# Kernel optimization log

Measured on AMD Instinct MI355X. Metric: run time of the kernel, lower is better.

The kernel has to match this reference:

```python
import jax, jax.numpy as jnp
import numpy as np


def setup_inputs() -> dict:
    key = jax.random.key(0)
    k1, k2, k3, k4 = jax.random.split(key, 4)
    B, S, D_IN, D_OUT = 4, 4096, 2048, 2048
    x = jax.random.normal(k1, (B, S, D_IN), dtype=jnp.float32)
    weight = jax.random.normal(k2, (D_OUT, D_IN), dtype=jnp.float32) * 0.02
    scale_weight = jax.random.uniform(k3, (D_OUT,), dtype=jnp.float32, minval=0.5, maxval=1.5)
    bias = jax.random.normal(k4, (D_OUT,), dtype=jnp.float32) * 0.02
    return {"x": x, "weight": weight, "scale_weight": scale_weight, "bias": bias}


def reference(x, weight, scale_weight, bias):
    # FPScaledLinear.forward: cast weight to compute dtype, apply per-out-feature
    # scale (scale_weight viewed as [out, 1]), then F.linear(x, w, b).
    w = weight * scale_weight[:, None]            # [out, in]
    out = jnp.einsum('bsi,oi->bso', x, w) + bias  # [B, S, out]
    return out
```

## Files before the change

### kernel.cpp

```cpp
#include <hip/hip_runtime.h>

typedef __attribute__((ext_vector_type(8))) __bf16 bf16x8;
typedef __attribute__((ext_vector_type(4))) float f32x4;
typedef __attribute__((ext_vector_type(8))) unsigned short ushort8;
typedef const __attribute__((address_space(1))) unsigned int gq_t;
typedef __attribute__((address_space(3))) unsigned int lq_t;

__device__ __forceinline__ unsigned short f2bf(float f) {
  unsigned int u = __builtin_bit_cast(unsigned int, f);
  u += 0x7fffu + ((u >> 16) & 1u);
  return (unsigned short)(u >> 16);
}

__global__ void cvt_xw_kernel(const float* __restrict__ x, const float* __restrict__ w,
                              const float* __restrict__ scale,
                              ushort8* __restrict__ xa, ushort8* __restrict__ wb,
                              int n8x, int n8w, int k8) {
  int stride = gridDim.x * blockDim.x;
  int total = n8x + n8w;
  for (int i = blockIdx.x * blockDim.x + threadIdx.x; i < total; i += stride) {
    if (i < n8x) {
      const float4* p = (const float4*)(x) + 2 * (size_t)i;
      float4 v0 = p[0], v1 = p[1];
      ushort8 r;
      r[0] = f2bf(v0.x); r[1] = f2bf(v0.y); r[2] = f2bf(v0.z); r[3] = f2bf(v0.w);
      r[4] = f2bf(v1.x); r[5] = f2bf(v1.y); r[6] = f2bf(v1.z); r[7] = f2bf(v1.w);
      xa[i] = r;
    } else {
      int j = i - n8x;
      float s = scale[j / k8];
      const float4* p = (const float4*)(w) + 2 * (size_t)j;
      float4 v0 = p[0], v1 = p[1];
      ushort8 r;
      r[0] = f2bf(v0.x * s); r[1] = f2bf(v0.y * s); r[2] = f2bf(v0.z * s); r[3] = f2bf(v0.w * s);
      r[4] = f2bf(v1.x * s); r[5] = f2bf(v1.y * s); r[6] = f2bf(v1.z * s); r[7] = f2bf(v1.w * s);
      wb[j] = r;
    }
  }
}


#define BARRIER asm volatile("s_barrier" ::: "memory")
#define WAITV4 asm volatile("s_waitcnt vmcnt(4)" ::: "memory")
#define WAITV0 asm volatile("s_waitcnt vmcnt(0)" ::: "memory")
#define GL(p, d) __builtin_amdgcn_global_load_lds((gq_t*)(p), (lq_t*)(d), 16, 0, 0)

#define QUAD(MH, BG, NHB)                                                                \
  do {                                                                                   \
    __builtin_amdgcn_s_setprio(1);                                                       \
    _Pragma("unroll") for (int k_ = 0; k_ < 2; ++k_) {                                   \
      _Pragma("unroll") for (int mm = 0; mm < 4; ++mm) {                                 \
        _Pragma("unroll") for (int nn = 0; nn < 2; ++nn) {                               \
          acc[(MH)*4 + mm][(NHB)*2 + nn] = __builtin_amdgcn_mfma_f32_16x16x32_bf16(      \
              af[mm][k_], BG[nn][k_], acc[(MH)*4 + mm][(NHB)*2 + nn], 0, 0, 0);          \
        }                                                                                \
      }                                                                                  \
    }                                                                                    \
    __builtin_amdgcn_s_setprio(0);                                                       \
  } while (0)

#define TILE_BODY(T, CB)                                                                 \
  do {                                                                                   \
    const int t_ = (T);                                                                  \
    char* cur = lds + (CB) * 65536;                                                      \
    char* oth = lds + (((CB) ^ 1)) * 65536;                                              \
                           \
    LDA(cur, 0);                                                                         \
    if (t_ + 1 < NT) { GL(bP0lo, oth + 32768 + dstT);                                    \
                       GL(bP0hi, oth + 32768 + 8192 + dstT); }                           \
    BARRIER; QUAD(0, bg0, 0);                                                            \
                                   \
    LDB1(cur);                                                                           \
    if (t_ + 1 < NT) { GL(aP1lo, oth + 16384 + dstT);                                    \
                       GL(aP1hi, oth + 16384 + 8192 + dstT); }                           \
    BARRIER; QUAD(0, bg1, 1);                                                            \
                                   \
    LDA(cur, 1);                                                                         \
    if (t_ + 2 < NT) { GL(aP0lo, cur + dstT);                                            \
                       GL(aP0hi, cur + 8192 + dstT); }                                   \
    BARRIER; QUAD(1, bg1, 1);                                                            \
       \
    if (t_ + 2 < NT) { GL(bP1lo, cur + 49152 + dstT);                                    \
                       GL(bP1hi, cur + 49152 + 8192 + dstT); }                           \
    if (t_ == NT - 2) { WAITV0; } else { WAITV4; }                                       \
    BARRIER; QUAD(1, bg0, 0);                                                            \
    if (t_ + 1 < NT) LDB0(oth);                                                          \
    aP0lo += 64; aP0hi += 64; aP1lo += 64; aP1hi += 64;                                  \
    bP0lo += 64; bP0hi += 64; bP1lo += 64; bP1hi += 64;                                  \
  } while (0)

__global__ __launch_bounds__(512, 2) void gemm256_8ph(
    const unsigned short* __restrict__ A, const unsigned short* __restrict__ B,
    const float* __restrict__ bias, float* __restrict__ C, int M, int N, int K) {
  extern __shared__ char lds[];

  const int nbn = N >> 8;
  const int nwg = (M >> 8) * nbn;
  int bid = blockIdx.x;
  if ((nwg & 7) == 0) {
    int q = nwg >> 3;
    bid = (bid & 7) * q + (bid >> 3);
  }
  const int bm = (bid / nbn) << 8;
  const int bn = (bid % nbn) << 8;

  const int tid = threadIdx.x;
  const int lane = tid & 63;
  const int wid = tid >> 6;
  const int wr = wid >> 2;
  const int wc = wid & 3;
  const int NT = K >> 6;
  const int dstT = tid * 16;

  const int colel = (((tid & 7) ^ ((tid >> 3) & 7)) << 3);
  const unsigned short* aBase = A + (size_t)(bm + (tid >> 3)) * K + colel;
  const unsigned short* bBase = B + (size_t)(bn + ((tid >> 8) << 6) + ((tid >> 3) & 31)) * K + colel;
  const unsigned short* aP0lo = aBase;
  const unsigned short* aP0hi = aBase + (size_t)128 * K;
  const unsigned short* aP1lo = aBase + (size_t)64 * K;
  const unsigned short* aP1hi = aBase + (size_t)192 * K;
  const unsigned short* bP0lo = bBase;
  const unsigned short* bP0hi = bBase + (size_t)128 * K;
  const unsigned short* bP1lo = bBase + (size_t)32 * K;
  const unsigned short* bP1hi = bBase + (size_t)160 * K;

  const int i15 = lane & 15;
  const int qg = lane >> 4;
  const int swz = (lane & 7) << 4;
  const int colp0 = (qg << 4) ^ swz;
  const int colp1 = ((qg << 4) | 64) ^ swz;
  const int aoff = wr * 8192 + i15 * 128;
  const int boff = 32768 + wc * 4096 + i15 * 128;

  f32x4 acc[8][4];
#pragma unroll
  for (int m = 0; m < 8; ++m)
#pragma unroll
    for (int n = 0; n < 4; ++n) acc[m][n] = (f32x4){0.f, 0.f, 0.f, 0.f};

  bf16x8 af[4][2];
  bf16x8 bg0[2][2];
  bf16x8 bg1[2][2];

  auto LDA = [&](const char* base, int mh) {
    const char* p = base + mh * 16384 + aoff;
#pragma unroll
    for (int mm = 0; mm < 4; ++mm) {
      af[mm][0] = *(const bf16x8*)(p + mm * 2048 + colp0);
      af[mm][1] = *(const bf16x8*)(p + mm * 2048 + colp1);
    }
  };
  auto LDB0 = [&](const char* base) {
    const char* p = base + boff;
#pragma unroll
    for (int nn = 0; nn < 2; ++nn) {
      bg0[nn][0] = *(const bf16x8*)(p + nn * 2048 + colp0);
      bg0[nn][1] = *(const bf16x8*)(p + nn * 2048 + colp1);
    }
  };
  auto LDB1 = [&](const char* base) {
    const char* p = base + 16384 + boff;
#pragma unroll
    for (int nn = 0; nn < 2; ++nn) {
      bg1[nn][0] = *(const bf16x8*)(p + nn * 2048 + colp0);
      bg1[nn][1] = *(const bf16x8*)(p + nn * 2048 + colp1);
    }
  };

  GL(aP0lo, lds + dstT);                     GL(aP0hi, lds + 8192 + dstT);
  GL(bP1lo, lds + 49152 + dstT);             GL(bP1hi, lds + 49152 + 8192 + dstT);
  GL(bP0lo, lds + 32768 + dstT);             GL(bP0hi, lds + 32768 + 8192 + dstT);
  GL(aP1lo, lds + 16384 + dstT);             GL(aP1hi, lds + 16384 + 8192 + dstT);
  GL(aP0lo + 64, lds + 65536 + dstT);        GL(aP0hi + 64, lds + 65536 + 8192 + dstT);
  GL(bP1lo + 64, lds + 65536 + 49152 + dstT);
  GL(bP1hi + 64, lds + 65536 + 49152 + 8192 + dstT);
  WAITV4;
  BARRIER;
  LDB0(lds);
  bP0lo += 64;  bP0hi += 64;  aP1lo += 64;  aP1hi += 64;
  aP0lo += 128; aP0hi += 128; bP1lo += 128; bP1hi += 128;

  for (int t = 0; t < NT; t += 2) {
    TILE_BODY(t, 0);
    TILE_BODY(t + 1, 1);
  }

  const int r0 = bm + wr * 128 + ((lane >> 4) << 2);
  const int c0 = bn + wc * 64 + (lane & 15);
  float bv[4];
#pragma unroll
  for (int n = 0; n < 4; ++n) bv[n] = bias[c0 + n * 16];
#pragma unroll
  for (int m = 0; m < 8; ++m) {
#pragma unroll
    for (int r = 0; r < 4; ++r) {
      float* crow = C + (size_t)(r0 + m * 16 + r) * N + c0;
#pragma unroll
      for (int n = 0; n < 4; ++n) crow[n * 16] = acc[m][n][r] + bv[n];
    }
  }
}

__global__ void gemm_fallback_kernel(const float* __restrict__ X, const float* __restrict__ W,
                                     const float* __restrict__ scale, const float* __restrict__ bias,
                                     float* __restrict__ out, int M, int N, int K) {
  __shared__ float as[64][33];
  __shared__ float bs[64][33];
  int tx = threadIdx.x & 15, ty = threadIdx.x >> 4;
  int brow = blockIdx.y * 64, bcol = blockIdx.x * 64;
  float acc[4][4] = {};
  for (int k0 = 0; k0 < K; k0 += 32) {
    int kw = (K - k0 < 32) ? (K - k0) : 32;
    for (int i = 0; i < 8; ++i) {
      int idx = (int)threadIdx.x + i * 256;
      int r = idx >> 5, c = idx & 31;
      int ga = brow + r, gb = bcol + r;
      as[r][c] = (ga < M && c < kw) ? X[(size_t)ga * K + k0 + c] : 0.f;
      bs[r][c] = (gb < N && c < kw) ? W[(size_t)gb * K + k0 + c] * scale[gb] : 0.f;
    }
    __syncthreads();
    for (int k = 0; k < 32; ++k)
#pragma unroll
      for (int i = 0; i < 4; ++i)
#pragma unroll
        for (int j = 0; j < 4; ++j)
          acc[i][j] += as[ty * 4 + i][k] * bs[tx * 4 + j][k];
    __syncthreads();
  }
  for (int i = 0; i < 4; ++i) {
    int r = brow + ty * 4 + i;
    if (r >= M) continue;
    for (int j = 0; j < 4; ++j) {
      int c = bcol + tx * 4 + j;
      if (c < N) out[(size_t)r * N + c] = acc[i][j] + bias[c];
    }
  }
}

extern "C" void kernel_launch(void* const* d_in, const int* in_sizes, int n_in,
                              void* d_out, int out_size, void* d_ws, size_t ws_size,
                              hipStream_t stream) {
  const float* x     = (const float*)d_in[0];
  const float* w     = (const float*)d_in[1];
  const float* scale = (const float*)d_in[2];
  const float* bias  = (const float*)d_in[3];
  float* out = (float*)d_out;

  const long N = in_sizes[2];
  const long K = in_sizes[1] / N;
  const long M = (long)in_sizes[0] / K;

  const size_t need = ((size_t)M * K + (size_t)N * K) * sizeof(unsigned short);
  const long NT = K / 64;
  const bool ok = (ws_size >= need) && (M % 256 == 0) && (N % 256 == 0) &&
                  (K % 128 == 0) && (NT >= 4);

  if (ok) {
    unsigned short* xa = (unsigned short*)d_ws;
    unsigned short* wb = xa + (size_t)M * K;
    int n8x = (int)((size_t)M * K / 8);
    int n8w = (int)((size_t)N * K / 8);
    cvt_xw_kernel<<<2048, 256, 0, stream>>>(x, w, scale, (ushort8*)xa, (ushort8*)wb,
                                            n8x, n8w, (int)(K / 8));

    (void)hipFuncSetAttribute((const void*)gemm256_8ph,
                              hipFuncAttributeMaxDynamicSharedMemorySize, 131072);
    int nwg = (int)((M / 256) * (N / 256));
    gemm256_8ph<<<nwg, 512, 131072, stream>>>(xa, wb, bias, out, (int)M, (int)N, (int)K);
  } else {
    dim3 grid((unsigned)((N + 63) / 64), (unsigned)((M + 63) / 64));
    gemm_fallback_kernel<<<grid, 256, 0, stream>>>(x, w, scale, bias, out, (int)M, (int)N, (int)K);
  }
}
```

Before: 164.6 us.

## Halve GEMM K-tile to 32 with new LDS swizzle and smaller shared memory

Shrinks the K depth per tile from 64 to 32, which halves the LDS buffer (64KB instead of 128KB) and the per-stage register fragments. It reworks the global-to-LDS load mapping and the read swizzle to fit the narrower tile, and lowers the outstanding-load wait count to match. The smaller LDS footprint is meant to let two workgroups fit per CU as the launch bounds ask. In exchange there are twice as many barriers and pipeline phases per unit of K, with less MFMA work between each sync.

```diff
diff --git a/kernel.cpp b/kernel.cpp
--- a/kernel.cpp
+++ b/kernel.cpp
@@ -41,19 +41,17 @@
 
 
 #define BARRIER asm volatile("s_barrier" ::: "memory")
-#define WAITV4 asm volatile("s_waitcnt vmcnt(4)" ::: "memory")
+#define WAITV2 asm volatile("s_waitcnt vmcnt(2)" ::: "memory")
 #define WAITV0 asm volatile("s_waitcnt vmcnt(0)" ::: "memory")
 #define GL(p, d) __builtin_amdgcn_global_load_lds((gq_t*)(p), (lq_t*)(d), 16, 0, 0)
 
 #define QUAD(MH, BG, NHB)                                                                \
   do {                                                                                   \
     __builtin_amdgcn_s_setprio(1);                                                       \
-    _Pragma("unroll") for (int k_ = 0; k_ < 2; ++k_) {                                   \
-      _Pragma("unroll") for (int mm = 0; mm < 4; ++mm) {                                 \
-        _Pragma("unroll") for (int nn = 0; nn < 2; ++nn) {                               \
-          acc[(MH)*4 + mm][(NHB)*2 + nn] = __builtin_amdgcn_mfma_f32_16x16x32_bf16(      \
-              af[mm][k_], BG[nn][k_], acc[(MH)*4 + mm][(NHB)*2 + nn], 0, 0, 0);          \
-        }                                                                                \
+    _Pragma("unroll") for (int mm = 0; mm < 4; ++mm) {                                   \
+      _Pragma("unroll") for (int nn = 0; nn < 2; ++nn) {                                 \
+        acc[(MH)*4 + mm][(NHB)*2 + nn] = __builtin_amdgcn_mfma_f32_16x16x32_bf16(        \
+            af[mm], BG[nn], acc[(MH)*4 + mm][(NHB)*2 + nn], 0, 0, 0);                    \
       }                                                                                  \
     }                                                                                    \
     __builtin_amdgcn_s_setprio(0);                                                       \
@@ -62,31 +60,26 @@
 #define TILE_BODY(T, CB)                                                                 \
   do {                                                                                   \
     const int t_ = (T);                                                                  \
-    char* cur = lds + (CB) * 65536;                                                      \
-    char* oth = lds + (((CB) ^ 1)) * 65536;                                              \
-                           \
+    char* cur = lds + (CB) * 32768;                                                      \
+    char* oth = lds + (((CB) ^ 1)) * 32768;                                              \
+                                                                                 \
     LDA(cur, 0);                                                                         \
-    if (t_ + 1 < NT) { GL(bP0lo, oth + 32768 + dstT);                                    \
-                       GL(bP0hi, oth + 32768 + 8192 + dstT); }                           \
+    if (t_ + 1 < NT) GL(bP0, oth + 16384 + dstT);                                        \
     BARRIER; QUAD(0, bg0, 0);                                                            \
-                                   \
+                                                                                 \
     LDB1(cur);                                                                           \
-    if (t_ + 1 < NT) { GL(aP1lo, oth + 16384 + dstT);                                    \
-                       GL(aP1hi, oth + 16384 + 8192 + dstT); }                           \
+    if (t_ + 1 < NT) GL(aP1, oth + 8192 + dstT);                                         \
     BARRIER; QUAD(0, bg1, 1);                                                            \
-                                   \
+                                                                                 \
     LDA(cur, 1);                                                                         \
-    if (t_ + 2 < NT) { GL(aP0lo, cur + dstT);                                            \
-                       GL(aP0hi, cur + 8192 + dstT); }                                   \
+    if (t_ + 2 < NT) GL(aP0, cur + dstT);                                                \
     BARRIER; QUAD(1, bg1, 1);                                                            \
-       \
-    if (t_ + 2 < NT) { GL(bP1lo, cur + 49152 + dstT);                                    \
-                       GL(bP1hi, cur + 49152 + 8192 + dstT); }                           \
-    if (t_ == NT - 2) { WAITV0; } else { WAITV4; }                                       \
+                                                                                 \
+    if (t_ + 2 < NT) GL(bP1, cur + 24576 + dstT);                                        \
+    if (t_ < NT - 2) { WAITV2; } else { WAITV0; }                                        \
     BARRIER; QUAD(1, bg0, 0);                                                            \
     if (t_ + 1 < NT) LDB0(oth);                                                          \
-    aP0lo += 64; aP0hi += 64; aP1lo += 64; aP1hi += 64;                                  \
-    bP0lo += 64; bP0hi += 64; bP1lo += 64; bP1hi += 64;                                  \
+    aP0 += 32; aP1 += 32; bP0 += 32; bP1 += 32;                                          \
   } while (0)
 
 __global__ __launch_bounds__(512, 2) void gemm256_8ph(
@@ -109,28 +102,20 @@
   const int wid = tid >> 6;
   const int wr = wid >> 2;
   const int wc = wid & 3;
-  const int NT = K >> 6;
+  const int NT = K >> 5;
   const int dstT = tid * 16;
 
-  const int colel = (((tid & 7) ^ ((tid >> 3) & 7)) << 3);
-  const unsigned short* aBase = A + (size_t)(bm + (tid >> 3)) * K + colel;
-  const unsigned short* bBase = B + (size_t)(bn + ((tid >> 8) << 6) + ((tid >> 3) & 31)) * K + colel;
-  const unsigned short* aP0lo = aBase;
-  const unsigned short* aP0hi = aBase + (size_t)128 * K;
-  const unsigned short* aP1lo = aBase + (size_t)64 * K;
-  const unsigned short* aP1hi = aBase + (size_t)192 * K;
-  const unsigned short* bP0lo = bBase;
-  const unsigned short* bP0hi = bBase + (size_t)128 * K;
-  const unsigned short* bP1lo = bBase + (size_t)32 * K;
-  const unsigned short* bP1hi = bBase + (size_t)160 * K;
+  const int colel = (((tid & 3) ^ ((tid >> 3) & 3)) << 3);
+  const unsigned short* aP0 =
+      A + (size_t)(bm + ((tid >> 8) << 7) + ((tid >> 2) & 63)) * K + colel;
+  const unsigned short* aP1 = aP0 + (size_t)64 * K;
+  const unsigned short* bP0 =
+      B + (size_t)(bn + ((tid >> 7) << 6) + ((tid >> 2) & 31)) * K + colel;
+  const unsigned short* bP1 = bP0 + (size_t)32 * K;
 
   const int i15 = lane & 15;
   const int qg = lane >> 4;
-  const int swz = (lane & 7) << 4;
-  const int colp0 = (qg << 4) ^ swz;
-  const int colp1 = ((qg << 4) | 64) ^ swz;
-  const int aoff = wr * 8192 + i15 * 128;
-  const int boff = 32768 + wc * 4096 + i15 * 128;
+  const int arow = ((i15 >> 1) << 7) + ((i15 & 1) << 6) + ((qg ^ ((i15 >> 1) & 3)) << 4);
 
   f32x4 acc[8][4];
 #pragma unroll
@@ -138,47 +123,37 @@
 #pragma unroll
     for (int n = 0; n < 4; ++n) acc[m][n] = (f32x4){0.f, 0.f, 0.f, 0.f};
 
-  bf16x8 af[4][2];
-  bf16x8 bg0[2][2];
-  bf16x8 bg1[2][2];
+  bf16x8 af[4];
+  bf16x8 bg0[2];
+  bf16x8 bg1[2];
 
   auto LDA = [&](const char* base, int mh) {
-    const char* p = base + mh * 16384 + aoff;
-#pragma unroll
-    for (int mm = 0; mm < 4; ++mm) {
-      af[mm][0] = *(const bf16x8*)(p + mm * 2048 + colp0);
-      af[mm][1] = *(const bf16x8*)(p + mm * 2048 + colp1);
-    }
+    const char* p = base + mh * 8192 + wr * 4096 + arow;
+#pragma unroll
+    for (int mm = 0; mm < 4; ++mm) af[mm] = *(const bf16x8*)(p + mm * 1024);
   };
   auto LDB0 = [&](const char* base) {
-    const char* p = base + boff;
-#pragma unroll
-    for (int nn = 0; nn < 2; ++nn) {
-      bg0[nn][0] = *(const bf16x8*)(p + nn * 2048 + colp0);
-      bg0[nn][1] = *(const bf16x8*)(p + nn * 2048 + colp1);
-    }
+    const char* p = base + 16384 + wc * 2048 + arow;
+#pragma unroll
+    for (int nn = 0; nn < 2; ++nn) bg0[nn] = *(const bf16x8*)(p + nn * 1024);
   };
   auto LDB1 = [&](const char* base) {
-    const char* p = base + 16384 + boff;
-#pragma unroll
-    for (int nn = 0; nn < 2; ++nn) {
-      bg1[nn][0] = *(const bf16x8*)(p + nn * 2048 + colp0);
-      bg1[nn][1] = *(const bf16x8*)(p + nn * 2048 + colp1);
-    }
+    const char* p = base + 24576 + wc * 2048 + arow;
+#pragma unroll
+    for (int nn = 0; nn < 2; ++nn) bg1[nn] = *(const bf16x8*)(p + nn * 1024);
   };
 
-  GL(aP0lo, lds + dstT);                     GL(aP0hi, lds + 8192 + dstT);
-  GL(bP1lo, lds + 49152 + dstT);             GL(bP1hi, lds + 49152 + 8192 + dstT);
-  GL(bP0lo, lds + 32768 + dstT);             GL(bP0hi, lds + 32768 + 8192 + dstT);
-  GL(aP1lo, lds + 16384 + dstT);             GL(aP1hi, lds + 16384 + 8192 + dstT);
-  GL(aP0lo + 64, lds + 65536 + dstT);        GL(aP0hi + 64, lds + 65536 + 8192 + dstT);
-  GL(bP1lo + 64, lds + 65536 + 49152 + dstT);
-  GL(bP1hi + 64, lds + 65536 + 49152 + 8192 + dstT);
-  WAITV4;
+  GL(aP0, lds + dstT);
+  GL(bP0, lds + 16384 + dstT);
+  GL(bP1, lds + 24576 + dstT);
+  GL(aP1, lds + 8192 + dstT);
+  GL(aP0 + 32, lds + 32768 + dstT);
+  GL(bP1 + 32, lds + 32768 + 24576 + dstT);
+  WAITV2;
   BARRIER;
   LDB0(lds);
-  bP0lo += 64;  bP0hi += 64;  aP1lo += 64;  aP1hi += 64;
-  aP0lo += 128; aP0hi += 128; bP1lo += 128; bP1hi += 128;
+  bP0 += 32; aP1 += 32;
+  aP0 += 64; bP1 += 64;
 
   for (int t = 0; t < NT; t += 2) {
     TILE_BODY(t, 0);
@@ -251,7 +226,7 @@
   const long M = (long)in_sizes[0] / K;
 
   const size_t need = ((size_t)M * K + (size_t)N * K) * sizeof(unsigned short);
-  const long NT = K / 64;
+  const long NT = K / 32;
   const bool ok = (ws_size >= need) && (M % 256 == 0) && (N % 256 == 0) &&
                   (K % 128 == 0) && (NT >= 4);
 
@@ -264,9 +239,9 @@
                                             n8x, n8w, (int)(K / 8));
 
     (void)hipFuncSetAttribute((const void*)gemm256_8ph,
-                              hipFuncAttributeMaxDynamicSharedMemorySize, 131072);
+                              hipFuncAttributeMaxDynamicSharedMemorySize, 65536);
     int nwg = (int)((M / 256) * (N / 256));
-    gemm256_8ph<<<nwg, 512, 131072, stream>>>(xa, wb, bias, out, (int)M, (int)N, (int)K);
+    gemm256_8ph<<<nwg, 512, 65536, stream>>>(xa, wb, bias, out, (int)M, (int)N, (int)K);
   } else {
     dim3 grid((unsigned)((N + 63) / 64), (unsigned)((M + 63) / 64));
     gemm_fallback_kernel<<<grid, 256, 0, stream>>>(x, w, scale, bias, out, (int)M, (int)N, (int)K);
```

Result: slower. 172.0 us (+4.5%).
